# Performance work log

Measured on AMD Instinct MI355X. Metric: run time of the kernel, lower is better.

The kernel has to match this reference:

```python
import jax, jax.numpy as jnp
import numpy as np
from jax.scipy.special import logsumexp

SIGMA = 1.0
EPSILON = 1.0
MAX_ITER = 10


def _gaussian_kernel(x, y, sigma):
    # x: (b, l, d), y: (b, k, d) -> (b, l, k) negative-kernel matrix exp(-||x-y||^2 / (2 sigma^2))
    outer = jnp.einsum('bld,bkd->blk', x, y)
    norm_x = jnp.sum(x * x, axis=2)
    norm_y = jnp.sum(y * y, axis=2)
    dist = (norm_x[:, :, None] + norm_y[:, None, :] - 2.0 * outer) / (2.0 * sigma ** 2)
    return jnp.exp(-jnp.maximum(dist, 0.0))


def setup_inputs() -> dict:
    key = jax.random.key(0)
    kx, ka, ky, kb = jax.random.split(key, 4)
    B, L, K, D = 8, 2048, 2048, 32
    return {
        'x': jax.random.normal(kx, (B, L, D), dtype=jnp.float32),
        'a': jax.random.normal(ka, (B, L), dtype=jnp.float32),
        'y': jax.random.normal(ky, (B, K, D), dtype=jnp.float32),
        'b': jax.random.normal(kb, (B, K), dtype=jnp.float32),
    }


def _sinkhorn_potentials(x, a, y, b):
    sg = jax.lax.stop_gradient
    # Kernel matrices (carry gradient wrt x, y); weights a, b are detached inside kernels.
    Kxx = _gaussian_kernel(x, x, SIGMA) / EPSILON + sg(a)[:, None, :]
    Kyx_base = _gaussian_kernel(y, x, SIGMA)
    Kyx = Kyx_base / EPSILON + sg(a)[:, None, :]
    Kxy = jnp.swapaxes(Kyx_base, 1, 2) / EPSILON + sg(b)[:, None, :]
    Kyy = _gaussian_kernel(y, y, SIGMA) / EPSILON + sg(b)[:, None, :]

    # Sinkhorn loop runs under no_grad in the original: stop-gradient kernels.
    Kxx_s, Kyx_s, Kxy_s, Kyy_s = sg(Kxx), sg(Kyx), sg(Kxy), sg(Kyy)

    def step(carry, _):
        fxx, fyx, fxy, fyy = carry
        # sequential (Gauss-Seidel) update order matches the torch dict order xx, yx, xy, yy
        fxx = 0.5 * fxx - 0.5 * logsumexp(Kxx_s + fxx[:, None, :], axis=2)
        fyx = 0.5 * fyx - 0.5 * logsumexp(Kyx_s + fxy[:, None, :], axis=2)  # uses old fxy
        fxy = 0.5 * fxy - 0.5 * logsumexp(Kxy_s + fyx[:, None, :], axis=2)  # uses new fyx
        fyy = 0.5 * fyy - 0.5 * logsumexp(Kyy_s + fyy[:, None, :], axis=2)
        return (fxx, fyx, fxy, fyy), None

    init = (jnp.zeros_like(a), jnp.zeros_like(b), jnp.zeros_like(a), jnp.zeros_like(b))
    (fxx, fyx, fxy, fyy), _ = jax.lax.scan(step, init, None, length=MAX_ITER)

    # Final differentiable extrapolation step (potentials are detached constants).
    fe_xx = -logsumexp(Kxx + fxx[:, None, :], axis=2)
    fe_yx = -logsumexp(Kyx + fxy[:, None, :], axis=2)
    fe_xy = -logsumexp(Kxy + fyx[:, None, :], axis=2)
    fe_yy = -logsumexp(Kyy + fyy[:, None, :], axis=2)
    f = fe_xy - fe_xx  # (b, l)
    g = fe_yx - fe_yy  # (b, k)
    return f, g


def reference(x, a, y, b):
    f, g = _sinkhorn_potentials(x, a, y, b)
    res = jnp.sum(f * jnp.exp(a), axis=1) + jnp.sum(g * jnp.exp(b), axis=1)
    return res * EPSILON  # (batch,)
```

## Files before the change

kernel.cpp:

```cpp
#include <hip/hip_runtime.h>
#include <hip/hip_bf16.h>

#define B_ 8
#define N_ 2048
#define D_ 32
#define RCAP 16
#define EM1_DIAG 1.7182818284590452f
#define M_   8.0f
#define EM_  2980.9579870417283f
#define L2E  1.4426950408889634f
#define LN2  0.6931471805599453f
#define MH_  (0.5f * M_ * L2E)

typedef __attribute__((ext_vector_type(8))) short short8;
typedef __attribute__((ext_vector_type(4))) float f32x4;

__global__ void setup_kernel(const float* __restrict__ x, const float* __restrict__ y,
                             unsigned short* __restrict__ xb, unsigned short* __restrict__ yb,
                             float* __restrict__ NX, float* __restrict__ NY,
                             int* __restrict__ csr_cnt)
{
    int t = blockIdx.x * 256 + threadIdx.x;
    const float* src = (t < 16384) ? x : y;
    unsigned short* dstb = (t < 16384) ? xb : yb;
    float* dstn = (t < 16384) ? NX : NY;
    int row = (t < 16384) ? t : (t - 16384);
    const float4* p = reinterpret_cast<const float4*>(src + (size_t)row * D_);
    float ss = 0.f;
    float4 v[8];
    #pragma unroll
    for (int k = 0; k < 8; k++) {
        v[k] = p[k];
        ss += v[k].x * v[k].x + v[k].y * v[k].y + v[k].z * v[k].z + v[k].w * v[k].w;
    }
    short8* dst8 = reinterpret_cast<short8*>(dstb + (size_t)row * D_);
    #pragma unroll
    for (int k = 0; k < 4; k++) {
        const float fv[8] = { v[2*k].x, v[2*k].y, v[2*k].z, v[2*k].w,
                              v[2*k+1].x, v[2*k+1].y, v[2*k+1].z, v[2*k+1].w };
        short8 o;
        #pragma unroll
        for (int e = 0; e < 8; e++) {
            __hip_bfloat16 h = __float2bfloat16(fv[e]);
            o[e] = *reinterpret_cast<const short*>(&h);
        }
        dst8[k] = o;
    }
    dstn[row] = ss * 0.5f;
    csr_cnt[2 * t] = 0;
    csr_cnt[2 * t + 1] = 0;
}

__global__ __launch_bounds__(256) void discover_kernel(
    const unsigned short* __restrict__ xb, const unsigned short* __restrict__ yb,
    const float* __restrict__ NX, const float* __restrict__ NY,
    int* __restrict__ csr_cnt, uint2* __restrict__ csr_ent)
{
    int m = blockIdx.x >> 10;
    int rem = blockIdx.x & 1023;
    int batch = rem >> 7;
    int rem2 = rem & 127;
    int rowblk = rem2 >> 2;
    int cchunk = rem2 & 3;
    const unsigned short* rd = (m == 0) ? xb : yb;
    const float*          rN = (m == 0) ? NX : NY;
    const unsigned short* cd = (m == 1) ? yb : xb;
    const float*          cN = (m == 1) ? NY : NX;

    const int tid = threadIdx.x, lane = tid & 63, wv = tid >> 6;
    const int r0 = rowblk * 64;
    const size_t rowbase = (size_t)batch * N_ + r0;

    short8 afrag[4];
    f32x4 cinit[4];
    #pragma unroll
    for (int g = 0; g < 4; g++) {
        afrag[g] = *reinterpret_cast<const short8*>(
            rd + (rowbase + g * 16 + (lane & 15)) * D_ + (lane >> 4) * 8);
        float4 nv = *reinterpret_cast<const float4*>(
            rN + rowbase + g * 16 + (lane >> 4) * 4);
        cinit[g][0] = -nv.x; cinit[g][1] = -nv.y; cinit[g][2] = -nv.z; cinit[g][3] = -nv.w;
    }
    const unsigned short* cdB = cd + (size_t)batch * N_ * D_;
    const float* cNB = cN + batch * N_;
    const int c0w = cchunk * 512 + wv * 128;

    unsigned mask = 0;
    #pragma unroll
    for (int cc = 0; cc < 8; ++cc) {
        int col = c0w + cc * 16 + (lane & 15);
        short8 bfrag = *reinterpret_cast<const short8*>(
            cdB + (size_t)col * D_ + (lane >> 4) * 8);
        float ny = cNB[col];
        f32x4 d[4];
        #pragma unroll
        for (int g = 0; g < 4; g++)
            d[g] = __builtin_amdgcn_mfma_f32_16x16x32_bf16(afrag[g], bfrag, cinit[g], 0, 0, 0);
        float m0 = fmaxf(fmaxf(d[0][0], d[0][1]), fmaxf(d[0][2], d[0][3]));
        float m1 = fmaxf(fmaxf(d[1][0], d[1][1]), fmaxf(d[1][2], d[1][3]));
        float m2 = fmaxf(fmaxf(d[2][0], d[2][1]), fmaxf(d[2][2], d[2][3]));
        float m3 = fmaxf(fmaxf(d[3][0], d[3][1]), fmaxf(d[3][2], d[3][3]));
        float mx = fmaxf(fmaxf(m0, m1), fmaxf(m2, m3));
        mask |= (__any(mx > ny - 10.0f) ? 1u : 0u) << cc;
    }

    auto push = [&](int T, int row, int colv, float em1) {
        size_t base = (size_t)(T * B_ + batch) * N_ + row;
        int idx = atomicAdd(&csr_cnt[base], 1);
        if (idx < RCAP)
            csr_ent[base * RCAP + idx] = make_uint2((unsigned)colv, __float_as_uint(em1));
    };
    while (mask) {
        int cc = __builtin_ctz(mask);
        mask &= mask - 1;
        int col = c0w + cc * 16 + (lane & 15);
        short8 bfrag = *reinterpret_cast<const short8*>(
            cdB + (size_t)col * D_ + (lane >> 4) * 8);
        float ny = cNB[col];
        f32x4 d[4];
        #pragma unroll
        for (int g = 0; g < 4; g++)
            d[g] = __builtin_amdgcn_mfma_f32_16x16x32_bf16(afrag[g], bfrag, cinit[g], 0, 0, 0);
        #pragma unroll
        for (int g = 0; g < 4; g++) {
            #pragma unroll
            for (int r = 0; r < 4; r++) {
                float dist = ny - d[g][r];
                if (dist < 10.0f) {
                    int i = r0 + g * 16 + (lane >> 4) * 4 + r;
                    if (m == 2) {
                        float em1 = __expf(__expf(-fmaxf(dist, 0.f))) - 1.0f;
                        push(2, i, col, em1);
                        push(3, col, i, em1);
                    } else if (i != col) {
                        float em1 = __expf(__expf(-fmaxf(dist, 0.f))) - 1.0f;
                        push(m, i, col, em1);
                    }
                }
            }
        }
    }
}

__global__ __launch_bounds__(1024) void sinkhorn_kernel(
    const float* __restrict__ a_in, const float* __restrict__ b_in,
    const int* __restrict__ csr_cnt, const uint2* __restrict__ csr_ent,
    float* __restrict__ out)
{
    __shared__ float evb[2][4][N_];
    __shared__ float Spart[2][4][16];
    __shared__ float resacc;

    const int batch = blockIdx.x;
    const int t = threadIdx.x, lane = t & 63, wv = t >> 6;

    int cnts[4][2];
    const uint2* ebase[4];
    uint2 ec[4][2][2];
    #pragma unroll
    for (int T = 0; T < 4; T++) {
        size_t bb = (size_t)(T * B_ + batch) * N_;
        ebase[T] = csr_ent + bb * (size_t)RCAP;
        #pragma unroll
        for (int q = 0; q < 2; q++) {
            int row = t + 1024 * q;
            int c = min(csr_cnt[bb + row], RCAP);
            cnts[T][q] = c;
            const uint2* E = ebase[T] + (size_t)row * RCAP;
            ec[T][q][0] = (c > 0) ? E[0] : make_uint2(0u, 0u);
            ec[T][q][1] = (c > 1) ? E[1] : make_uint2(0u, 0u);
        }
    }
    float AW[2], BW[2];
    float F0[2] = {0.f, 0.f}, F1[2] = {0.f, 0.f}, F2[2] = {0.f, 0.f}, F3[2] = {0.f, 0.f};
    #pragma unroll
    for (int q = 0; q < 2; q++) {
        int j = t + 1024 * q;
        AW[q] = (a_in[batch * N_ + j] - M_) * L2E;
        BW[q] = (b_in[batch * N_ + j] - M_) * L2E;
    }
    if (t == 0) resacc = 0.f;
    __syncthreads();

    auto gath = [&](int T, int q, const float* evbuf) -> float {
        int c = cnts[T][q];
        float g = 0.f;
        if (c > 0) g += evbuf[ec[T][q][0].x] * __uint_as_float(ec[T][q][0].y);
        if (c > 1) g += evbuf[ec[T][q][1].x] * __uint_as_float(ec[T][q][1].y);
        if (__builtin_expect(c > 2, 0)) {
            const uint2* E = ebase[T] + (size_t)(t + 1024 * q) * RCAP;
            for (int k = 2; k < c; ++k)
                g += evbuf[E[k].x] * __uint_as_float(E[k].y);
        }
        return g;
    };
    auto wpart = [&](float v, float* slot) {
        #pragma unroll
        for (int off = 1; off < 64; off <<= 1) v += __shfl_xor(v, off, 64);
        if (lane == 0) *slot = v;
    };
    auto tree16 = [](const float* r) -> float {
        return (((r[0] + r[1]) + (r[2] + r[3])) + ((r[4] + r[5]) + (r[6] + r[7])))
             + (((r[8] + r[9]) + (r[10] + r[11])) + ((r[12] + r[13]) + (r[14] + r[15])));
    };

    auto stageA = [&](int s) {
        const int p = s & 1;
        float e0q[2], e2q[2];
        float s0 = 0.f, s1 = 0.f, s2 = 0.f;
        #pragma unroll
        for (int q = 0; q < 2; q++) {
            int j = t + 1024 * q;
            float e0 = __builtin_amdgcn_exp2f(AW[q] + F0[q]); evb[p][0][j] = e0; e0q[q] = e0; s0 += e0;
            float e1 = __builtin_amdgcn_exp2f(AW[q] + F2[q]); evb[p][1][j] = e1;              s1 += e1;
            float e2 = __builtin_amdgcn_exp2f(BW[q] + F3[q]); evb[p][2][j] = e2; e2q[q] = e2; s2 += e2;
        }
        wpart(s0, &Spart[p][0][wv]);
        wpart(s1, &Spart[p][1][wv]);
        wpart(s2, &Spart[p][2][wv]);
        __syncthreads();
        float S0 = tree16(Spart[p][0]);
        float S1 = tree16(Spart[p][1]);
        float S2 = tree16(Spart[p][2]);
        #pragma unroll
        for (int q = 0; q < 2; q++) {
            float g0 = gath(0, q, evb[p][0]);
            float g1 = gath(2, q, evb[p][1]);
            float g2 = gath(1, q, evb[p][2]);
            float lg0 = __builtin_amdgcn_logf(S0 + fmaf(e0q[q], EM1_DIAG, g0));
            float lg1 = __builtin_amdgcn_logf(S1 + g1);
            float lg2 = __builtin_amdgcn_logf(S2 + fmaf(e2q[q], EM1_DIAG, g2));
            F0[q] = fmaf(0.5f, F0[q], -fmaf(0.5f, lg0, MH_));
            F1[q] = fmaf(0.5f, F1[q], -fmaf(0.5f, lg1, MH_));
            F3[q] = fmaf(0.5f, F3[q], -fmaf(0.5f, lg2, MH_));
        }
    };

    auto stageB = [&](int s) {
        const int p = s & 1;
        float sB = 0.f;
        #pragma unroll
        for (int q = 0; q < 2; q++) {
            int j = t + 1024 * q;
            float e = __builtin_amdgcn_exp2f(BW[q] + F1[q]); evb[p][0][j] = e; sB += e;
        }
        wpart(sB, &Spart[p][0][wv]);
        __syncthreads();
        float S = tree16(Spart[p][0]);
        #pragma unroll
        for (int q = 0; q < 2; q++) {
            float g = gath(3, q, evb[p][0]);
            F2[q] = fmaf(0.5f, F2[q], -fmaf(0.5f, __builtin_amdgcn_logf(S + g), MH_));
        }
    };

    int s = 0;
    for (int it = 0; it < 10; ++it) {
        stageA(s); ++s;
        stageB(s); ++s;
    }

    {
        const int p = s & 1;
        float e0q[2], e3q[2];
        float s0 = 0.f, s1 = 0.f, s2 = 0.f, s3 = 0.f;
        #pragma unroll
        for (int q = 0; q < 2; q++) {
            int j = t + 1024 * q;
            float e0 = __builtin_amdgcn_exp2f(AW[q] + F0[q]); evb[p][0][j] = e0; e0q[q] = e0; s0 += e0;
            float e1 = __builtin_amdgcn_exp2f(AW[q] + F2[q]); evb[p][1][j] = e1;              s1 += e1;
            float e2 = __builtin_amdgcn_exp2f(BW[q] + F1[q]); evb[p][2][j] = e2;              s2 += e2;
            float e3 = __builtin_amdgcn_exp2f(BW[q] + F3[q]); evb[p][3][j] = e3; e3q[q] = e3; s3 += e3;
        }
        wpart(s0, &Spart[p][0][wv]);
        wpart(s1, &Spart[p][1][wv]);
        wpart(s2, &Spart[p][2][wv]);
        wpart(s3, &Spart[p][3][wv]);
        __syncthreads();
        float S0 = tree16(Spart[p][0]), S1 = tree16(Spart[p][1]);
        float S2 = tree16(Spart[p][2]), S3 = tree16(Spart[p][3]);
        float ctr = 0.f;
        #pragma unroll
        for (int q = 0; q < 2; q++) {
            float lg0 = __builtin_amdgcn_logf(S0 + fmaf(e0q[q], EM1_DIAG, gath(0, q, evb[p][0])));
            float lg1 = __builtin_amdgcn_logf(S1 + gath(2, q, evb[p][1]));
            float lg2 = __builtin_amdgcn_logf(S2 + gath(3, q, evb[p][2]));
            float lg3 = __builtin_amdgcn_logf(S3 + fmaf(e3q[q], EM1_DIAG, gath(1, q, evb[p][3])));
            float ea = __builtin_amdgcn_exp2f(AW[q]);
            float eb = __builtin_amdgcn_exp2f(BW[q]);
            ctr += (lg0 - lg2) * ea + (lg3 - lg1) * eb;
        }
        ctr *= (LN2 * EM_);
        #pragma unroll
        for (int off = 1; off < 64; off <<= 1) ctr += __shfl_xor(ctr, off, 64);
        if (lane == 0) atomicAdd(&resacc, ctr);
        __syncthreads();
        if (t == 0) out[batch] = resacc;
    }
}

extern "C" void kernel_launch(void* const* d_in, const int* in_sizes, int n_in,
                              void* d_out, int out_size, void* d_ws, size_t ws_size,
                              hipStream_t stream)
{
    const float* x = (const float*)d_in[0];
    const float* a = (const float*)d_in[1];
    const float* y = (const float*)d_in[2];
    const float* b = (const float*)d_in[3];
    float* out = (float*)d_out;

    char* ws = (char*)d_ws;
    size_t o = 0;
    unsigned short* xb = (unsigned short*)(ws + o); o += (size_t)B_ * N_ * D_ * 2;
    unsigned short* yb = (unsigned short*)(ws + o); o += (size_t)B_ * N_ * D_ * 2;
    float* NX = (float*)(ws + o); o += (size_t)B_ * N_ * 4;
    float* NY = (float*)(ws + o); o += (size_t)B_ * N_ * 4;
    int* csr_cnt = (int*)(ws + o); o += (size_t)4 * B_ * N_ * 4;
    uint2* csr_ent = (uint2*)(ws + o); o += (size_t)4 * B_ * N_ * RCAP * 8;

    setup_kernel<<<128, 256, 0, stream>>>(x, y, xb, yb, NX, NY, csr_cnt);
    discover_kernel<<<3 * 1024, 256, 0, stream>>>(xb, yb, NX, NY, csr_cnt, csr_ent);
    sinkhorn_kernel<<<B_, 1024, 0, stream>>>(a, b, csr_cnt, csr_ent, out);
}
```

Baseline: 176.2 us.

## Split Sinkhorn chains across three independent wavefronts without block barriers

The 1024-thread sinkhorn block is replaced by three wavefronts per batch. One runs the coupled xy/yx chain and the other two run the independent xx and yy self-chains, each wave holding 32 potentials per lane in registers. Reductions use wave shuffles only, so the per-stage __syncthreads and shared partial-sum trees are removed. In exchange, far fewer threads do the exp/log and sparse-gather work, and CSR entries are read from global memory every iteration instead of being cached in registers.

Measured after the change: 505.0 us. 187% more time.

```diff
diff --git a/kernel.cpp b/kernel.cpp
--- a/kernel.cpp
+++ b/kernel.cpp
@@ -142,161 +142,142 @@
     }
 }
 
-__global__ __launch_bounds__(1024) void sinkhorn_kernel(
+__global__ __launch_bounds__(192) void sinkhorn_kernel(
     const float* __restrict__ a_in, const float* __restrict__ b_in,
     const int* __restrict__ csr_cnt, const uint2* __restrict__ csr_ent,
     float* __restrict__ out)
 {
-    __shared__ float evb[2][4][N_];
-    __shared__ float Spart[2][4][16];
-    __shared__ float resacc;
+    __shared__ float evb[3][N_];
+    __shared__ float slot[3];
 
     const int batch = blockIdx.x;
-    const int t = threadIdx.x, lane = t & 63, wv = t >> 6;
-
-    int cnts[4][2];
-    const uint2* ebase[4];
-    uint2 ec[4][2][2];
-    #pragma unroll
-    for (int T = 0; T < 4; T++) {
-        size_t bb = (size_t)(T * B_ + batch) * N_;
-        ebase[T] = csr_ent + bb * (size_t)RCAP;
-        #pragma unroll
-        for (int q = 0; q < 2; q++) {
-            int row = t + 1024 * q;
-            int c = min(csr_cnt[bb + row], RCAP);
-            cnts[T][q] = c;
-            const uint2* E = ebase[T] + (size_t)row * RCAP;
-            ec[T][q][0] = (c > 0) ? E[0] : make_uint2(0u, 0u);
-            ec[T][q][1] = (c > 1) ? E[1] : make_uint2(0u, 0u);
+    const int t = threadIdx.x, wv = t >> 6, lane = t & 63;
+    float partial = 0.f;
+
+    if (wv == 0) {
+        float AW[32], BW[32], FY[32], FX[32];
+        unsigned cp2[4] = {0,0,0,0}, cp3[4] = {0,0,0,0};
+        const size_t bb2 = (size_t)(2 * B_ + batch) * N_;
+        const size_t bb3 = (size_t)(3 * B_ + batch) * N_;
+        #pragma unroll
+        for (int k = 0; k < 32; k++) {
+            int j = lane + 64 * k;
+            AW[k] = (a_in[batch * N_ + j] - M_) * L2E;
+            BW[k] = (b_in[batch * N_ + j] - M_) * L2E;
+            FY[k] = 0.f; FX[k] = 0.f;
+            cp2[k >> 3] |= (unsigned)min(csr_cnt[bb2 + j], 15) << ((k & 7) * 4);
+            cp3[k >> 3] |= (unsigned)min(csr_cnt[bb3 + j], 15) << ((k & 7) * 4);
         }
-    }
-    float AW[2], BW[2];
-    float F0[2] = {0.f, 0.f}, F1[2] = {0.f, 0.f}, F2[2] = {0.f, 0.f}, F3[2] = {0.f, 0.f};
-    #pragma unroll
-    for (int q = 0; q < 2; q++) {
-        int j = t + 1024 * q;
-        AW[q] = (a_in[batch * N_ + j] - M_) * L2E;
-        BW[q] = (b_in[batch * N_ + j] - M_) * L2E;
-    }
-    if (t == 0) resacc = 0.f;
+        const uint2* E2 = csr_ent + bb2 * (size_t)RCAP;
+        const uint2* E3 = csr_ent + bb3 * (size_t)RCAP;
+        float* ev = evb[0];
+
+        auto stageYX = [&](bool ext) {
+            float s = 0.f;
+            #pragma unroll
+            for (int k = 0; k < 32; k++) {
+                float e = __builtin_amdgcn_exp2f(AW[k] + FX[k]);
+                ev[lane + 64 * k] = e; s += e;
+            }
+            #pragma unroll
+            for (int off = 1; off < 64; off <<= 1) s += __shfl_xor(s, off, 64);
+            #pragma unroll
+            for (int k = 0; k < 32; k++) {
+                float g = 0.f;
+                int nib = (cp2[k >> 3] >> ((k & 7) * 4)) & 15;
+                if (nib) {
+                    const uint2* E = E2 + (size_t)(lane + 64 * k) * RCAP;
+                    g += ev[E[0].x] * __uint_as_float(E[0].y);
+                    if (nib > 1) g += ev[E[1].x] * __uint_as_float(E[1].y);
+                    if (nib > 2)
+                        for (int e2 = 2; e2 < nib; ++e2)
+                            g += ev[E[e2].x] * __uint_as_float(E[e2].y);
+                }
+                float lg = __builtin_amdgcn_logf(s + g);
+                if (!ext) FY[k] = fmaf(0.5f, FY[k], -fmaf(0.5f, lg, MH_));
+                else      partial -= lg * __builtin_amdgcn_exp2f(BW[k]);
+            }
+        };
+        auto stageXY = [&](bool ext) {
+            float s = 0.f;
+            #pragma unroll
+            for (int k = 0; k < 32; k++) {
+                float e = __builtin_amdgcn_exp2f(BW[k] + FY[k]);
+                ev[lane + 64 * k] = e; s += e;
+            }
+            #pragma unroll
+            for (int off = 1; off < 64; off <<= 1) s += __shfl_xor(s, off, 64);
+            #pragma unroll
+            for (int k = 0; k < 32; k++) {
+                float g = 0.f;
+                int nib = (cp3[k >> 3] >> ((k & 7) * 4)) & 15;
+                if (nib) {
+                    const uint2* E = E3 + (size_t)(lane + 64 * k) * RCAP;
+                    g += ev[E[0].x] * __uint_as_float(E[0].y);
+                    if (nib > 1) g += ev[E[1].x] * __uint_as_float(E[1].y);
+                    if (nib > 2)
+                        for (int e2 = 2; e2 < nib; ++e2)
+                            g += ev[E[e2].x] * __uint_as_float(E[e2].y);
+                }
+                float lg = __builtin_amdgcn_logf(s + g);
+                if (!ext) FX[k] = fmaf(0.5f, FX[k], -fmaf(0.5f, lg, MH_));
+                else      partial -= lg * __builtin_amdgcn_exp2f(AW[k]);
+            }
+        };
+        for (int it = 0; it < 10; ++it) { stageYX(false); stageXY(false); }
+        stageYX(true);
+        stageXY(true);
+    } else {
+        const int T = (wv == 1) ? 0 : 1;
+        const float* w_in = (wv == 1) ? a_in : b_in;
+        float W[32], F[32], e[32];
+        unsigned cp[4] = {0,0,0,0};
+        const size_t bb = (size_t)(T * B_ + batch) * N_;
+        #pragma unroll
+        for (int k = 0; k < 32; k++) {
+            int j = lane + 64 * k;
+            W[k] = (w_in[batch * N_ + j] - M_) * L2E;
+            F[k] = 0.f;
+            cp[k >> 3] |= (unsigned)min(csr_cnt[bb + j], 15) << ((k & 7) * 4);
+        }
+        const uint2* Eb = csr_ent + bb * (size_t)RCAP;
+        float* ev = evb[wv];
+
+        auto stage = [&](bool ext) {
+            float s = 0.f;
+            #pragma unroll
+            for (int k = 0; k < 32; k++) {
+                e[k] = __builtin_amdgcn_exp2f(W[k] + F[k]);
+                ev[lane + 64 * k] = e[k]; s += e[k];
+            }
+            #pragma unroll
+            for (int off = 1; off < 64; off <<= 1) s += __shfl_xor(s, off, 64);
+            #pragma unroll
+            for (int k = 0; k < 32; k++) {
+                float g = e[k] * EM1_DIAG;
+                int nib = (cp[k >> 3] >> ((k & 7) * 4)) & 15;
+                if (nib) {
+                    const uint2* E = Eb + (size_t)(lane + 64 * k) * RCAP;
+                    g += ev[E[0].x] * __uint_as_float(E[0].y);
+                    if (nib > 1) g += ev[E[1].x] * __uint_as_float(E[1].y);
+                    if (nib > 2)
+                        for (int e2 = 2; e2 < nib; ++e2)
+                            g += ev[E[e2].x] * __uint_as_float(E[e2].y);
+                }
+                float lg = __builtin_amdgcn_logf(s + g);
+                if (!ext) F[k] = fmaf(0.5f, F[k], -fmaf(0.5f, lg, MH_));
+                else      partial += lg * __builtin_amdgcn_exp2f(W[k]);
+            }
+        };
+        for (int it = 0; it < 10; ++it) stage(false);
+        stage(true);
+    }
+
+    #pragma unroll
+    for (int off = 1; off < 64; off <<= 1) partial += __shfl_xor(partial, off, 64);
+    if (lane == 0) slot[wv] = partial;
     __syncthreads();
-
-    auto gath = [&](int T, int q, const float* evbuf) -> float {
-        int c = cnts[T][q];
-        float g = 0.f;
-        if (c > 0) g += evbuf[ec[T][q][0].x] * __uint_as_float(ec[T][q][0].y);
-        if (c > 1) g += evbuf[ec[T][q][1].x] * __uint_as_float(ec[T][q][1].y);
-        if (__builtin_expect(c > 2, 0)) {
-            const uint2* E = ebase[T] + (size_t)(t + 1024 * q) * RCAP;
-            for (int k = 2; k < c; ++k)
-                g += evbuf[E[k].x] * __uint_as_float(E[k].y);
-        }
-        return g;
-    };
-    auto wpart = [&](float v, float* slot) {
-        #pragma unroll
-        for (int off = 1; off < 64; off <<= 1) v += __shfl_xor(v, off, 64);
-        if (lane == 0) *slot = v;
-    };
-    auto tree16 = [](const float* r) -> float {
-        return (((r[0] + r[1]) + (r[2] + r[3])) + ((r[4] + r[5]) + (r[6] + r[7])))
-             + (((r[8] + r[9]) + (r[10] + r[11])) + ((r[12] + r[13]) + (r[14] + r[15])));
-    };
-
-    auto stageA = [&](int s) {
-        const int p = s & 1;
-        float e0q[2], e2q[2];
-        float s0 = 0.f, s1 = 0.f, s2 = 0.f;
-        #pragma unroll
-        for (int q = 0; q < 2; q++) {
-            int j = t + 1024 * q;
-            float e0 = __builtin_amdgcn_exp2f(AW[q] + F0[q]); evb[p][0][j] = e0; e0q[q] = e0; s0 += e0;
-            float e1 = __builtin_amdgcn_exp2f(AW[q] + F2[q]); evb[p][1][j] = e1;              s1 += e1;
-            float e2 = __builtin_amdgcn_exp2f(BW[q] + F3[q]); evb[p][2][j] = e2; e2q[q] = e2; s2 += e2;
-        }
-        wpart(s0, &Spart[p][0][wv]);
-        wpart(s1, &Spart[p][1][wv]);
-        wpart(s2, &Spart[p][2][wv]);
-        __syncthreads();
-        float S0 = tree16(Spart[p][0]);
-        float S1 = tree16(Spart[p][1]);
-        float S2 = tree16(Spart[p][2]);
-        #pragma unroll
-        for (int q = 0; q < 2; q++) {
-            float g0 = gath(0, q, evb[p][0]);
-            float g1 = gath(2, q, evb[p][1]);
-            float g2 = gath(1, q, evb[p][2]);
-            float lg0 = __builtin_amdgcn_logf(S0 + fmaf(e0q[q], EM1_DIAG, g0));
-            float lg1 = __builtin_amdgcn_logf(S1 + g1);
-            float lg2 = __builtin_amdgcn_logf(S2 + fmaf(e2q[q], EM1_DIAG, g2));
-            F0[q] = fmaf(0.5f, F0[q], -fmaf(0.5f, lg0, MH_));
-            F1[q] = fmaf(0.5f, F1[q], -fmaf(0.5f, lg1, MH_));
-            F3[q] = fmaf(0.5f, F3[q], -fmaf(0.5f, lg2, MH_));
-        }
-    };
-
-    auto stageB = [&](int s) {
-        const int p = s & 1;
-        float sB = 0.f;
-        #pragma unroll
-        for (int q = 0; q < 2; q++) {
-            int j = t + 1024 * q;
-            float e = __builtin_amdgcn_exp2f(BW[q] + F1[q]); evb[p][0][j] = e; sB += e;
-        }
-        wpart(sB, &Spart[p][0][wv]);
-        __syncthreads();
-        float S = tree16(Spart[p][0]);
-        #pragma unroll
-        for (int q = 0; q < 2; q++) {
-            float g = gath(3, q, evb[p][0]);
-            F2[q] = fmaf(0.5f, F2[q], -fmaf(0.5f, __builtin_amdgcn_logf(S + g), MH_));
-        }
-    };
-
-    int s = 0;
-    for (int it = 0; it < 10; ++it) {
-        stageA(s); ++s;
-        stageB(s); ++s;
-    }
-
-    {
-        const int p = s & 1;
-        float e0q[2], e3q[2];
-        float s0 = 0.f, s1 = 0.f, s2 = 0.f, s3 = 0.f;
-        #pragma unroll
-        for (int q = 0; q < 2; q++) {
-            int j = t + 1024 * q;
-            float e0 = __builtin_amdgcn_exp2f(AW[q] + F0[q]); evb[p][0][j] = e0; e0q[q] = e0; s0 += e0;
-            float e1 = __builtin_amdgcn_exp2f(AW[q] + F2[q]); evb[p][1][j] = e1;              s1 += e1;
-            float e2 = __builtin_amdgcn_exp2f(BW[q] + F1[q]); evb[p][2][j] = e2;              s2 += e2;
-            float e3 = __builtin_amdgcn_exp2f(BW[q] + F3[q]); evb[p][3][j] = e3; e3q[q] = e3; s3 += e3;
-        }
-        wpart(s0, &Spart[p][0][wv]);
-        wpart(s1, &Spart[p][1][wv]);
-        wpart(s2, &Spart[p][2][wv]);
-        wpart(s3, &Spart[p][3][wv]);
-        __syncthreads();
-        float S0 = tree16(Spart[p][0]), S1 = tree16(Spart[p][1]);
-        float S2 = tree16(Spart[p][2]), S3 = tree16(Spart[p][3]);
-        float ctr = 0.f;
-        #pragma unroll
-        for (int q = 0; q < 2; q++) {
-            float lg0 = __builtin_amdgcn_logf(S0 + fmaf(e0q[q], EM1_DIAG, gath(0, q, evb[p][0])));
-            float lg1 = __builtin_amdgcn_logf(S1 + gath(2, q, evb[p][1]));
-            float lg2 = __builtin_amdgcn_logf(S2 + gath(3, q, evb[p][2]));
-            float lg3 = __builtin_amdgcn_logf(S3 + fmaf(e3q[q], EM1_DIAG, gath(1, q, evb[p][3])));
-            float ea = __builtin_amdgcn_exp2f(AW[q]);
-            float eb = __builtin_amdgcn_exp2f(BW[q]);
-            ctr += (lg0 - lg2) * ea + (lg3 - lg1) * eb;
-        }
-        ctr *= (LN2 * EM_);
-        #pragma unroll
-        for (int off = 1; off < 64; off <<= 1) ctr += __shfl_xor(ctr, off, 64);
-        if (lane == 0) atomicAdd(&resacc, ctr);
-        __syncthreads();
-        if (t == 0) out[batch] = resacc;
-    }
+    if (t == 0) out[batch] = (slot[0] + slot[1] + slot[2]) * (LN2 * EM_);
 }
 
 extern "C" void kernel_launch(void* const* d_in, const int* in_sizes, int n_in,
@@ -320,5 +301,5 @@
 
     setup_kernel<<<128, 256, 0, stream>>>(x, y, xb, yb, NX, NY, csr_cnt);
     discover_kernel<<<3 * 1024, 256, 0, stream>>>(xb, yb, NX, NY, csr_cnt, csr_ent);
-    sinkhorn_kernel<<<B_, 1024, 0, stream>>>(a, b, csr_cnt, csr_ent, out);
+    sinkhorn_kernel<<<B_, 192, 0, stream>>>(a, b, csr_cnt, csr_ent, out);
 }
```
